# Performance work log

Hardware: AMD Instinct MI355X
Metric: run time of the kernel (lower is better)

The kernel has to match this reference:

```python
import jax, jax.numpy as jnp
import numpy as np

N_EMBD = 1024
N_HEAD = 16
B, T = 2, 2048


def setup_inputs() -> dict:
    key = jax.random.key(0)
    k1, k2, k3 = jax.random.split(key, 3)
    scale = 1.0 / np.sqrt(N_EMBD)
    x = jax.random.normal(k1, (B, T, N_EMBD), dtype=jnp.float32)
    W_qkv = jax.random.normal(k2, (N_EMBD, 3 * N_EMBD), dtype=jnp.float32) * scale
    b_qkv = jnp.zeros((3 * N_EMBD,), dtype=jnp.float32)
    W_proj = jax.random.normal(k3, (N_EMBD, N_EMBD), dtype=jnp.float32) * scale
    b_proj = jnp.zeros((N_EMBD,), dtype=jnp.float32)
    return {"x": x, "W_qkv": W_qkv, "b_qkv": b_qkv, "W_proj": W_proj, "b_proj": b_proj}


def reference(x, W_qkv, b_qkv, W_proj, b_proj):
    Bx, Tx, C = x.shape
    H = N_HEAD
    D = C // H  # head_size
    qkv = x @ W_qkv + b_qkv  # [B,T,3C]
    Q, K, V = jnp.split(qkv, 3, axis=2)
    # [B,T,C] -> [B,H,T,D]
    Q = Q.reshape(Bx, Tx, H, D).transpose(0, 2, 1, 3)
    K = K.reshape(Bx, Tx, H, D).transpose(0, 2, 1, 3)
    V = V.reshape(Bx, Tx, H, D).transpose(0, 2, 1, 3)
    scores = jnp.einsum("bhqd,bhkd->bhqk", Q, K) / jnp.sqrt(jnp.float32(D))
    causal = jnp.tril(jnp.ones((Tx, Tx), dtype=bool))
    scores = jnp.where(causal, scores, jnp.float32(-jnp.inf))
    weights = jax.nn.softmax(scores, axis=-1)
    out = jnp.einsum("bhqk,bhkd->bhqd", weights, V)  # [B,H,T,D]
    out = out.transpose(0, 2, 1, 3).reshape(Bx, Tx, C)
    return out @ W_proj + b_proj
```

## Files before the change

kernel.cpp:

```cpp
#include <hip/hip_runtime.h>
#include <hip/hip_bf16.h>
#include <math.h>

#define BB 2
#define TT 2048
#define CC 1024
#define HH 16
#define DD 64
#define C3 3072
#define BT 4096

typedef __attribute__((ext_vector_type(8))) short short8;
typedef __attribute__((ext_vector_type(8))) unsigned short ushort8;
typedef __attribute__((ext_vector_type(4))) unsigned short ushort4v;
typedef __attribute__((ext_vector_type(4))) float floatx4;

__device__ __forceinline__ unsigned short f2b(float f) {
    union { float f; unsigned int u; } v; v.f = f;
    unsigned int u = v.u;
    unsigned int r = (u + 0x7fffu + ((u >> 16) & 1u)) >> 16;
    return (unsigned short)r;
}
__device__ __forceinline__ unsigned short f2b_fast(float f) {
    unsigned int u = __builtin_bit_cast(unsigned int, f);
    return (unsigned short)((u + 0x8000u) >> 16);
}

__device__ __forceinline__ void store_out(unsigned short* p, float v) { *p = f2b(v); }
__device__ __forceinline__ void store_out(float* p, float v) { *p = v; }

__device__ __forceinline__ void async16(const unsigned short* g, unsigned short* lds) {
    __builtin_amdgcn_global_load_lds(
        (const __attribute__((address_space(1))) unsigned int*)g,
        (__attribute__((address_space(3))) unsigned int*)lds, 16, 0, 0);
}

__global__ __launch_bounds__(256) void prep_kernel(
    const float* __restrict__ x, unsigned short* __restrict__ xb,
    const float* __restrict__ Wqkv, const float* __restrict__ Wproj,
    unsigned short* __restrict__ Wqkv_t, unsigned short* __restrict__ Wproj_t)
{
    __shared__ float tile[64 * 65];
    const int tid = threadIdx.x;
    const int bid = blockIdx.x;

    if (bid < 2048) {
        int i = bid * 256 + tid;
        const float4 v0 = *(const float4*)&x[(size_t)i * 8];
        const float4 v1 = *(const float4*)&x[(size_t)i * 8 + 4];
        ushort8 pk;
        pk[0] = f2b(v0.x); pk[1] = f2b(v0.y); pk[2] = f2b(v0.z); pk[3] = f2b(v0.w);
        pk[4] = f2b(v1.x); pk[5] = f2b(v1.y); pk[6] = f2b(v1.z); pk[7] = f2b(v1.w);
        *(ushort8*)&xb[(size_t)i * 8] = pk;
        return;
    }

    const int xt = bid - 2048;
    const int cxt = xt & 63;
    const int r0  = (xt >> 6) * 64;
    const float* src; unsigned short* dst; int Ccols, c0;
    if (cxt < 48) { src = Wqkv;  dst = Wqkv_t;  Ccols = C3; c0 = cxt * 64; }
    else          { src = Wproj; dst = Wproj_t; Ccols = CC; c0 = (cxt - 48) * 64; }
#pragma unroll
    for (int it = 0; it < 4; it++) {
        int idx = it * 256 + tid;
        int row = idx >> 4;
        int c4  = idx & 15;
        float4 v = *(const float4*)&src[(size_t)(r0 + row) * Ccols + c0 + c4 * 4];
        tile[row * 65 + c4 * 4 + 0] = v.x;
        tile[row * 65 + c4 * 4 + 1] = v.y;
        tile[row * 65 + c4 * 4 + 2] = v.z;
        tile[row * 65 + c4 * 4 + 3] = v.w;
    }
    __syncthreads();
#pragma unroll
    for (int it = 0; it < 2; it++) {
        int idx = it * 256 + tid;
        int orow = idx >> 3;
        int o8   = idx & 7;
        ushort8 pk;
#pragma unroll
        for (int j = 0; j < 8; j++) pk[j] = f2b(tile[(o8 * 8 + j) * 65 + orow]);
        *(ushort8*)&dst[(size_t)(c0 + orow) * CC + r0 + o8 * 8] = pk;
    }
}

template <typename OUT_T, bool FRAG>
__global__ __launch_bounds__(256) void gemm_bt_kernel(
    const unsigned short* __restrict__ A, const unsigned short* __restrict__ Bm,
    const float* __restrict__ bias, OUT_T* __restrict__ Cmat,
    unsigned short* __restrict__ Qf, unsigned short* __restrict__ Kf,
    unsigned short* __restrict__ Vf,
    int M, int N, int K, float qscale)
{
    __shared__ __align__(16) unsigned short sA[128 * 64];
    __shared__ __align__(16) unsigned short sB[128 * 64];

    const int tid = threadIdx.x;
    const int lane16 = tid & 15, quad = (tid & 63) >> 4;
    const int w = tid >> 6;
    const int wm = w >> 1, wn = w & 1;
    const int m0 = blockIdx.y * 128, n0 = blockIdx.x * 128;
    const int lx = lane16 & 7;

    floatx4 acc[4][4] = {};

    for (int kt = 0; kt < K; kt += 64) {
#pragma unroll
        for (int it = 0; it < 4; it++) {
            int idx = it * 256 + tid;
            int row = idx >> 3;
            int c8m = (idx & 7) ^ (row & 7);
            int wslot = it * 256 + (tid & 192);
            async16(&A[(size_t)(m0 + row) * K + kt + c8m * 8], &sA[wslot * 8]);
            async16(&Bm[(size_t)(n0 + row) * K + kt + c8m * 8], &sB[wslot * 8]);
        }
        __syncthreads();
#pragma unroll
        for (int ks = 0; ks < 64; ks += 32) {
            const int slot = ((ks >> 3) + quad) ^ lx;
            short8 af[4], bf[4];
#pragma unroll
            for (int t = 0; t < 4; t++) {
                af[t] = *(const short8*)&sA[(wm * 64 + t * 16 + lane16) * 64 + slot * 8];
                bf[t] = *(const short8*)&sB[(wn * 64 + t * 16 + lane16) * 64 + slot * 8];
            }
#pragma unroll
            for (int mt = 0; mt < 4; mt++)
#pragma unroll
                for (int nt = 0; nt < 4; nt++)
                    acc[mt][nt] = __builtin_amdgcn_mfma_f32_16x16x32_bf16(
                        af[mt], bf[nt], acc[mt][nt], 0, 0, 0);
        }
        __syncthreads();
    }

#pragma unroll
    for (int mt = 0; mt < 4; mt++) {
#pragma unroll
        for (int nt = 0; nt < 4; nt++) {
            int col = n0 + wn * 64 + nt * 16 + lane16;
            float bv = bias[col];
            int row0 = m0 + wm * 64 + mt * 16 + quad * 4;
            if (!FRAG) {
#pragma unroll
                for (int r = 0; r < 4; r++)
                    store_out(&Cmat[(size_t)(row0 + r) * N + col], acc[mt][nt][r] + bv);
            } else {
                const int breg = row0 >> 11;
                const int tok0 = row0 & (TT - 1);
                if (col < CC) {
                    int h = col >> 6, d = col & 63;
                    int bh = breg * HH + h;
                    size_t base = ((size_t)(bh * 128 + (tok0 >> 4)) * 2 + (d >> 5)) * 512
                                + ((d >> 3) & 3) * 128 + (tok0 & 15) * 8 + (d & 7);
#pragma unroll
                    for (int r = 0; r < 4; r++)
                        Qf[base + r * 8] = f2b((acc[mt][nt][r] + bv) * qscale);
                } else if (col < 2 * CC) {
                    int c = col - CC;
                    int h = c >> 6, d = c & 63;
                    int bh = breg * HH + h;
                    size_t base = ((size_t)(bh * 128 + (tok0 >> 4)) * 2 + (d >> 5)) * 512
                                + ((d >> 3) & 3) * 128 + (tok0 & 15) * 8 + (d & 7);
#pragma unroll
                    for (int r = 0; r < 4; r++)
                        Kf[base + r * 8] = f2b(acc[mt][nt][r] + bv);
                } else {
                    int c = col - 2 * CC;
                    int h = c >> 6, d = c & 63;
                    int bh = breg * HH + h;
                    size_t base = ((size_t)(bh * 64 + (tok0 >> 5)) * 4 + (d >> 4)) * 512
                                + (((tok0 >> 2) & 3) * 16 + (d & 15)) * 8
                                + ((tok0 >> 4) & 1) * 4;
                    ushort4v pk;
#pragma unroll
                    for (int r = 0; r < 4; r++) pk[r] = f2b(acc[mt][nt][r] + bv);
                    *(ushort4v*)&Vf[base] = pk;
                }
            }
        }
    }
}

__global__ __launch_bounds__(256) void attn_mfma_kernel(
    const unsigned short* __restrict__ Qf, const unsigned short* __restrict__ Kf,
    const unsigned short* __restrict__ Vf, unsigned short* __restrict__ att)
{
    __shared__ __align__(16) unsigned short Ks[2][8 * 512];
    __shared__ __align__(16) unsigned short Vs[2][8 * 512];

    const int tid = threadIdx.x;
    const int l = tid & 63;
    const int w = tid >> 6;
    const int lane16 = l & 15, quad = l >> 4;
    const int bh = blockIdx.x;
    const int b = bh >> 4, h = bh & 15;

    const int y = blockIdx.y;
    const int gcu = y & 7, s = y >> 3;
    const int p = 8 * s + ((s & 1) ? (7 - gcu) : gcu);
    const int q0 = p * 64;
    const int qw = q0 + w * 16;

    const unsigned short* Qb  = Qf + (size_t)bh * 131072 + l * 8;
    const unsigned short* KbT = Kf + (size_t)bh * 131072;
    const unsigned short* VbT = Vf + (size_t)bh * 131072;

    short8 qf0 = *(const short8*)&Qb[(size_t)((qw >> 4) * 2 + 0) * 512];
    short8 qf1 = *(const short8*)&Qb[(size_t)((qw >> 4) * 2 + 1) * 512];

    floatx4 O[4] = {};
    float ps = 0.f;
    const int ntiles = p + 1;
    const int qrow = qw + lane16;

    auto stage = [&](int tt, int buf) {
#pragma unroll
        for (int s4 = 0; s4 < 4; s4++) {
            int c = s4 * 4 + w;
            if (c < 8)
                async16(&KbT[((size_t)tt * 8 + c) * 512 + l * 8], &Ks[buf][c * 512]);
            else
                async16(&VbT[((size_t)tt * 8 + (c - 8)) * 512 + l * 8], &Vs[buf][(c - 8) * 512]);
        }
    };

    stage(0, 0);
    __syncthreads();

    int cur = 0;
    for (int t = 0; t < ntiles; ++t) {
        if (t + 1 < ntiles) stage(t + 1, cur ^ 1);

        short8 kf[8];
#pragma unroll
        for (int i = 0; i < 8; i++)
            kf[i] = *(const short8*)&Ks[cur][i * 512 + l * 8];

        const bool last = (t == ntiles - 1);
        short8 pa[2];
#pragma unroll
        for (int nt = 0; nt < 4; nt++) {
            floatx4 s4v = {};
            s4v = __builtin_amdgcn_mfma_f32_16x16x32_bf16(kf[nt * 2 + 0], qf0, s4v, 0, 0, 0);
            s4v = __builtin_amdgcn_mfma_f32_16x16x32_bf16(kf[nt * 2 + 1], qf1, s4v, 0, 0, 0);
#pragma unroll
            for (int r = 0; r < 4; r++) {
                float v = s4v[r];
                if (last) {
                    int key = t * 64 + nt * 16 + quad * 4 + r;
                    if (key > qrow) v = -1e30f;
                }
                float pe = __builtin_amdgcn_exp2f(v);
                ps += pe;
                pa[nt >> 1][(nt & 1) * 4 + r] = (short)f2b_fast(pe);
            }
        }

#pragma unroll
        for (int kc = 0; kc < 2; kc++) {
            short8 vfr[4];
#pragma unroll
            for (int i = 0; i < 4; i++)
                vfr[i] = *(const short8*)&Vs[cur][(kc * 4 + i) * 512 + l * 8];
#pragma unroll
            for (int dt = 0; dt < 4; dt++)
                O[dt] = __builtin_amdgcn_mfma_f32_16x16x32_bf16(
                    pa[kc], vfr[dt], O[dt], 0, 0, 0);
        }

        __syncthreads();
        cur ^= 1;
    }

    ps += __shfl_xor(ps, 16, 64);
    ps += __shfl_xor(ps, 32, 64);

    unsigned short* ob = att + ((size_t)(b * TT) + qw) * CC + h * DD;
#pragma unroll
    for (int r = 0; r < 4; r++) {
        float rl = 1.0f / __shfl(ps, quad * 4 + r, 16);
        int q = quad * 4 + r;
#pragma unroll
        for (int dt = 0; dt < 4; dt++)
            ob[(size_t)q * CC + dt * 16 + lane16] = f2b(O[dt][r] * rl);
    }
}

extern "C" void kernel_launch(void* const* d_in, const int* in_sizes, int n_in,
                              void* d_out, int out_size, void* d_ws, size_t ws_size,
                              hipStream_t stream) {
    const float* x     = (const float*)d_in[0];
    const float* Wqkv  = (const float*)d_in[1];
    const float* bqkv  = (const float*)d_in[2];
    const float* Wproj = (const float*)d_in[3];
    const float* bproj = (const float*)d_in[4];
    float* out = (float*)d_out;

    const size_t FRAG_ELEMS = (size_t)128 * 2 * 512;
    unsigned short* xb      = (unsigned short*)d_ws;
    unsigned short* Qf      = xb + (size_t)BT * CC;
    unsigned short* Kf      = Qf + (size_t)BB * HH * FRAG_ELEMS;
    unsigned short* Vf      = Kf + (size_t)BB * HH * FRAG_ELEMS;
    unsigned short* Wqkv_t  = Vf + (size_t)BB * HH * FRAG_ELEMS;
    unsigned short* Wproj_t = Wqkv_t + (size_t)C3 * CC;
    unsigned short* att_b   = Wproj_t + (size_t)CC * CC;

    prep_kernel<<<3072, 256, 0, stream>>>(x, xb, Wqkv, Wproj, Wqkv_t, Wproj_t);

    {
        dim3 grid(C3 / 128, BT / 128);
        gemm_bt_kernel<unsigned short, true><<<grid, 256, 0, stream>>>(
            xb, Wqkv_t, bqkv, (unsigned short*)nullptr, Qf, Kf, Vf,
            BT, C3, CC, 0.125f * 1.44269504f);
    }
    {
        dim3 grid(BB * HH, 32);
        attn_mfma_kernel<<<grid, 256, 0, stream>>>(Qf, Kf, Vf, att_b);
    }
    {
        dim3 grid(CC / 128, BT / 128);
        gemm_bt_kernel<float, false><<<grid, 256, 0, stream>>>(
            att_b, Wproj_t, bproj, out, nullptr, nullptr, nullptr,
            BT, CC, CC, 1.0f);
    }
}
```

Baseline: 173.2 us.

## Replace QKV GEMM with 256x256-tile double-buffered async-copy kernel

Measured after the change: 174.1 us. Within noise of the previous version (+0.5%).

```diff
diff --git a/kernel.cpp b/kernel.cpp
--- a/kernel.cpp
+++ b/kernel.cpp
@@ -85,13 +85,11 @@
     }
 }
 
-template <typename OUT_T, bool FRAG>
+template <typename OUT_T>
 __global__ __launch_bounds__(256) void gemm_bt_kernel(
     const unsigned short* __restrict__ A, const unsigned short* __restrict__ Bm,
     const float* __restrict__ bias, OUT_T* __restrict__ Cmat,
-    unsigned short* __restrict__ Qf, unsigned short* __restrict__ Kf,
-    unsigned short* __restrict__ Vf,
-    int M, int N, int K, float qscale)
+    int M, int N, int K)
 {
     __shared__ __align__(16) unsigned short sA[128 * 64];
     __shared__ __align__(16) unsigned short sB[128 * 64];
@@ -142,42 +140,165 @@
             int col = n0 + wn * 64 + nt * 16 + lane16;
             float bv = bias[col];
             int row0 = m0 + wm * 64 + mt * 16 + quad * 4;
-            if (!FRAG) {
+#pragma unroll
+            for (int r = 0; r < 4; r++)
+                store_out(&Cmat[(size_t)(row0 + r) * N + col], acc[mt][nt][r] + bv);
+        }
+    }
+}
+
+__global__ __launch_bounds__(512, 2) void gemm256_frag_kernel(
+    const unsigned short* __restrict__ A, const unsigned short* __restrict__ Bm,
+    const float* __restrict__ bias,
+    unsigned short* __restrict__ Qf, unsigned short* __restrict__ Kf,
+    unsigned short* __restrict__ Vf, float qscale)
+{
+    __shared__ __align__(16) unsigned short sAB[65536];
+
+    const int K = CC;
+    const int NT = K / 64;
+    const int tid = threadIdx.x;
+    const int lane16 = tid & 15, quad = (tid & 63) >> 4;
+    const int w = tid >> 6;
+    const int wm = w >> 2, wn = w & 3;
+    const int m0 = blockIdx.y * 256, n0 = blockIdx.x * 256;
+    const int lx = lane16 & 7;
+    const int wbase = tid & 0x1C0;
+
+    floatx4 acc[8][4] = {};
+
+    auto stage = [&](int tn, int q, unsigned short* dA, unsigned short* dB) {
+        int idx = q * 512 + tid;
+        int row = idx >> 3;
+        int cc  = (idx & 7) ^ (row & 7);
+        size_t koff = (size_t)tn * 64 + cc * 8;
+        int dchunk = (q * 512 + wbase) * 8;
+        async16(&A[(size_t)(m0 + row) * K + koff], &dA[dchunk]);
+        async16(&Bm[(size_t)(n0 + row) * K + koff], &dB[dchunk]);
+    };
+
+    {
+        unsigned short* dA = &sAB[0];
+        unsigned short* dB = &sAB[32768];
+#pragma unroll
+        for (int q = 0; q < 4; q++) stage(0, q, dA, dB);
+    }
+
+    for (int t = 0; t < NT; ++t) {
+        const int pi = t & 1;
+        unsigned short* sAc = &sAB[pi * 16384];
+        unsigned short* sBc = &sAB[32768 + pi * 16384];
+        unsigned short* sAn = &sAB[(pi ^ 1) * 16384];
+        unsigned short* sBn = &sAB[32768 + (pi ^ 1) * 16384];
+        const bool pre = (t + 1 < NT);
+
+        if (pre) {
+            stage(t + 1, 0, sAn, sBn);
+            asm volatile("s_waitcnt vmcnt(2)" ::: "memory");
+        } else {
+            asm volatile("s_waitcnt vmcnt(0)" ::: "memory");
+        }
+        __builtin_amdgcn_s_barrier();
+
+        short8 bf[4][2];
+#pragma unroll
+        for (int nt = 0; nt < 4; nt++)
+#pragma unroll
+            for (int ks = 0; ks < 2; ks++) {
+                int r = wn * 64 + nt * 16 + lane16;
+                int slot = (ks * 4 + quad) ^ lx;
+                bf[nt][ks] = *(const short8*)&sBc[r * 64 + slot * 8];
+            }
+        {
+            short8 af[2][2];
+#pragma unroll
+            for (int m2 = 0; m2 < 2; m2++)
+#pragma unroll
+                for (int ks = 0; ks < 2; ks++) {
+                    int r = wm * 128 + m2 * 16 + lane16;
+                    int slot = (ks * 4 + quad) ^ lx;
+                    af[m2][ks] = *(const short8*)&sAc[r * 64 + slot * 8];
+                }
+            asm volatile("s_waitcnt lgkmcnt(0)" ::: "memory");
+            __builtin_amdgcn_sched_barrier(0);
+            __builtin_amdgcn_s_setprio(1);
+#pragma unroll
+            for (int m2 = 0; m2 < 2; m2++)
+#pragma unroll
+                for (int nt = 0; nt < 4; nt++)
+#pragma unroll
+                    for (int ks = 0; ks < 2; ks++)
+                        acc[m2][nt] = __builtin_amdgcn_mfma_f32_16x16x32_bf16(
+                            af[m2][ks], bf[nt][ks], acc[m2][nt], 0, 0, 0);
+            __builtin_amdgcn_s_setprio(0);
+        }
+
+#pragma unroll
+        for (int q = 1; q < 4; q++) {
+            if (pre) stage(t + 1, q, sAn, sBn);
+            short8 af[2][2];
+#pragma unroll
+            for (int m2 = 0; m2 < 2; m2++)
+#pragma unroll
+                for (int ks = 0; ks < 2; ks++) {
+                    int r = wm * 128 + (2 * q + m2) * 16 + lane16;
+                    int slot = (ks * 4 + quad) ^ lx;
+                    af[m2][ks] = *(const short8*)&sAc[r * 64 + slot * 8];
+                }
+            asm volatile("s_waitcnt lgkmcnt(0)" ::: "memory");
+            __builtin_amdgcn_sched_barrier(0);
+            __builtin_amdgcn_s_setprio(1);
+#pragma unroll
+            for (int m2 = 0; m2 < 2; m2++)
+#pragma unroll
+                for (int nt = 0; nt < 4; nt++)
+#pragma unroll
+                    for (int ks = 0; ks < 2; ks++)
+                        acc[2 * q + m2][nt] = __builtin_amdgcn_mfma_f32_16x16x32_bf16(
+                            af[m2][ks], bf[nt][ks], acc[2 * q + m2][nt], 0, 0, 0);
+            __builtin_amdgcn_s_setprio(0);
+        }
+
+        __builtin_amdgcn_s_barrier();
+    }
+
+#pragma unroll
+    for (int mt = 0; mt < 8; mt++) {
+#pragma unroll
+        for (int nt = 0; nt < 4; nt++) {
+            int col = n0 + wn * 64 + nt * 16 + lane16;
+            float bv = bias[col];
+            int row0 = m0 + wm * 128 + mt * 16 + quad * 4;
+            const int breg = row0 >> 11;
+            const int tok0 = row0 & (TT - 1);
+            if (col < CC) {
+                int h = col >> 6, d = col & 63;
+                int bh = breg * HH + h;
+                size_t base = ((size_t)(bh * 128 + (tok0 >> 4)) * 2 + (d >> 5)) * 512
+                            + ((d >> 3) & 3) * 128 + (tok0 & 15) * 8 + (d & 7);
 #pragma unroll
                 for (int r = 0; r < 4; r++)
-                    store_out(&Cmat[(size_t)(row0 + r) * N + col], acc[mt][nt][r] + bv);
+                    Qf[base + r * 8] = f2b((acc[mt][nt][r] + bv) * qscale);
+            } else if (col < 2 * CC) {
+                int c = col - CC;
+                int h = c >> 6, d = c & 63;
+                int bh = breg * HH + h;
+                size_t base = ((size_t)(bh * 128 + (tok0 >> 4)) * 2 + (d >> 5)) * 512
+                            + ((d >> 3) & 3) * 128 + (tok0 & 15) * 8 + (d & 7);
+#pragma unroll
+                for (int r = 0; r < 4; r++)
+                    Kf[base + r * 8] = f2b(acc[mt][nt][r] + bv);
             } else {
-                const int breg = row0 >> 11;
-                const int tok0 = row0 & (TT - 1);
-                if (col < CC) {
-                    int h = col >> 6, d = col & 63;
-                    int bh = breg * HH + h;
-                    size_t base = ((size_t)(bh * 128 + (tok0 >> 4)) * 2 + (d >> 5)) * 512
-                                + ((d >> 3) & 3) * 128 + (tok0 & 15) * 8 + (d & 7);
-#pragma unroll
-                    for (int r = 0; r < 4; r++)
-                        Qf[base + r * 8] = f2b((acc[mt][nt][r] + bv) * qscale);
-                } else if (col < 2 * CC) {
-                    int c = col - CC;
-                    int h = c >> 6, d = c & 63;
-                    int bh = breg * HH + h;
-                    size_t base = ((size_t)(bh * 128 + (tok0 >> 4)) * 2 + (d >> 5)) * 512
-                                + ((d >> 3) & 3) * 128 + (tok0 & 15) * 8 + (d & 7);
-#pragma unroll
-                    for (int r = 0; r < 4; r++)
-                        Kf[base + r * 8] = f2b(acc[mt][nt][r] + bv);
-                } else {
-                    int c = col - 2 * CC;
-                    int h = c >> 6, d = c & 63;
-                    int bh = breg * HH + h;
-                    size_t base = ((size_t)(bh * 64 + (tok0 >> 5)) * 4 + (d >> 4)) * 512
-                                + (((tok0 >> 2) & 3) * 16 + (d & 15)) * 8
-                                + ((tok0 >> 4) & 1) * 4;
-                    ushort4v pk;
-#pragma unroll
-                    for (int r = 0; r < 4; r++) pk[r] = f2b(acc[mt][nt][r] + bv);
-                    *(ushort4v*)&Vf[base] = pk;
-                }
+                int c = col - 2 * CC;
+                int h = c >> 6, d = c & 63;
+                int bh = breg * HH + h;
+                size_t base = ((size_t)(bh * 64 + (tok0 >> 5)) * 4 + (d >> 4)) * 512
+                            + (((tok0 >> 2) & 3) * 16 + (d & 15)) * 8
+                            + ((tok0 >> 4) & 1) * 4;
+                ushort4v pk;
+#pragma unroll
+                for (int r = 0; r < 4; r++) pk[r] = f2b(acc[mt][nt][r] + bv);
+                *(ushort4v*)&Vf[base] = pk;
             }
         }
     }
@@ -310,10 +431,9 @@
     prep_kernel<<<3072, 256, 0, stream>>>(x, xb, Wqkv, Wproj, Wqkv_t, Wproj_t);
 
     {
-        dim3 grid(C3 / 128, BT / 128);
-        gemm_bt_kernel<unsigned short, true><<<grid, 256, 0, stream>>>(
-            xb, Wqkv_t, bqkv, (unsigned short*)nullptr, Qf, Kf, Vf,
-            BT, C3, CC, 0.125f * 1.44269504f);
+        dim3 grid(C3 / 256, BT / 256);
+        gemm256_frag_kernel<<<grid, 512, 0, stream>>>(
+            xb, Wqkv_t, bqkv, Qf, Kf, Vf, 0.125f * 1.44269504f);
     }
     {
         dim3 grid(BB * HH, 32);
@@ -321,8 +441,7 @@
     }
     {
         dim3 grid(CC / 128, BT / 128);
-        gemm_bt_kernel<float, false><<<grid, 256, 0, stream>>>(
-            att_b, Wproj_t, bproj, out, nullptr, nullptr, nullptr,
-            BT, CC, CC, 1.0f);
-    }
-}
+        gemm_bt_kernel<float><<<grid, 256, 0, stream>>>(
+            att_b, Wproj_t, bproj, out, BT, CC, CC);
+    }
+}
```
